# Performance work log

Measured on AMD Instinct MI355X. Metric: run time of the kernel, lower is better.

## Reference

```python
import jax, jax.numpy as jnp
import numpy as np

LOG2 = float(np.log(2.0))
CUTOFF = 10.0
N, E, H, F, G = 50000, 800000, 64, 64, 50


def ssp(x):
    # ShiftedSoftplus
    return jax.nn.softplus(x) - LOG2


def setup_inputs() -> dict:
    key = jax.random.key(0)
    ks = jax.random.split(key, 20)
    s = 0.05
    inp = {
        'x0': jax.random.normal(ks[0], (N, H), jnp.float32),
        'x1': jax.random.normal(ks[1], (N, H), jnp.float32),
        'edge_index0': jax.random.randint(ks[2], (2, E), 0, N, jnp.int32),
        'edge_index1': jax.random.randint(ks[3], (2, E), 0, N, jnp.int32),
        'edge_weight0': jax.random.uniform(ks[4], (E,), jnp.float32) * CUTOFF,
        'edge_weight1': jax.random.uniform(ks[5], (E,), jnp.float32) * CUTOFF,
        'edge_attr0': jax.random.uniform(ks[6], (E, G), jnp.float32),
        'edge_attr1': jax.random.uniform(ks[7], (E, G), jnp.float32),
        # shared filter MLP (num_gaussians -> num_filters -> num_filters)
        'mlp_w1': jax.random.normal(ks[8], (G, F), jnp.float32) * s,
        'mlp_b1': jnp.zeros((F,), jnp.float32),
        'mlp_w2': jax.random.normal(ks[9], (F, F), jnp.float32) * s,
        'mlp_b2': jnp.zeros((F,), jnp.float32),
        # per-edge-type CFConv lin1 (H->F, no bias) and lin2 (F->H, bias)
        'lin1_w0': jax.random.normal(ks[10], (H, F), jnp.float32) * s,
        'lin2_w0': jax.random.normal(ks[11], (F, H), jnp.float32) * s,
        'lin2_b0': jnp.zeros((H,), jnp.float32),
        'lin1_w1': jax.random.normal(ks[12], (H, F), jnp.float32) * s,
        'lin2_w1': jax.random.normal(ks[13], (F, H), jnp.float32) * s,
        'lin2_b1': jnp.zeros((H,), jnp.float32),
        # trailing shared linear H->H
        'lin_w': jax.random.normal(ks[14], (H, H), jnp.float32) * s,
        'lin_b': jnp.zeros((H,), jnp.float32),
    }
    return inp


def cfconv(x, ei, ew, ea, l1w, l2w, l2b, mw1, mb1, mw2, mb2):
    # cosine cutoff on distances
    C = 0.5 * (jnp.cos(ew * (jnp.pi / CUTOFF)) + 1.0)  # [E]
    # filter MLP on RBF edge attrs: Linear -> SSP -> Linear
    W = (ssp(ea @ mw1 + mb1) @ mw2 + mb2) * C[:, None]  # [E,F]
    xs = x @ l1w                                        # [N,F]
    msg = xs[ei[0]] * W                                 # gather src, modulate
    agg = jax.ops.segment_sum(msg, ei[1], num_segments=x.shape[0])  # scatter-sum to dst
    return agg @ l2w + l2b                              # [N,H]


def reference(x0, x1, edge_index0, edge_index1, edge_weight0, edge_weight1,
              edge_attr0, edge_attr1, mlp_w1, mlp_b1, mlp_w2, mlp_b2,
              lin1_w0, lin2_w0, lin2_b0, lin1_w1, lin2_w1, lin2_b1,
              lin_w, lin_b):
    h0 = cfconv(x0, edge_index0, edge_weight0, edge_attr0,
                lin1_w0, lin2_w0, lin2_b0, mlp_w1, mlp_b1, mlp_w2, mlp_b2)
    h1 = cfconv(x1, edge_index1, edge_weight1, edge_attr1,
                lin1_w1, lin2_w1, lin2_b1, mlp_w1, mlp_b1, mlp_w2, mlp_b2)
    out0 = ssp(h0) @ lin_w + lin_b
    out1 = ssp(h1) @ lin_w + lin_b
    return out0, out1
```

## Files before the change

kernel.cpp:

```cpp
#include <hip/hip_runtime.h>
#include <math.h>

#define HD 64
#define GD 50
#define HALF 32
#define PAD 36
#define EPW 64
#define WPB 2

__device__ __forceinline__ float ssp_f(float x) {
    float ax = __builtin_fabsf(x);
    float e  = __expf(-ax);
    float sp = fmaxf(x, 0.0f) + __logf(1.0f + e);
    return sp - 0.69314718055994531f;
}

__global__ void __launch_bounds__(256) xs_kernel(
        const float* __restrict__ xA, const float* __restrict__ xB,
        const float* __restrict__ wA, const float* __restrict__ wB,
        float* __restrict__ xsA, float* __restrict__ xsB,
        float* __restrict__ aggA, float* __restrict__ aggB,
        int NA, int NB) {
    const int t = blockIdx.y;
    const float* x   = t ? xB : xA;
    const float* w   = t ? wB : wA;
    float* xs  = t ? xsB : xsA;
    float* agg = t ? aggB : aggA;
    const int N = t ? NB : NA;

    int wv = threadIdx.x >> 6;
    int j  = threadIdx.x & 63;
    int n  = blockIdx.x * 4 + wv;
    __shared__ float xr[4][64];
    if (n < N) xr[wv][j] = x[(size_t)n * HD + j];
    __syncthreads();
    if (n >= N) return;
    float acc = 0.0f;
#pragma unroll
    for (int k = 0; k < HD; ++k)
        acc = fmaf(xr[wv][k], w[k * HD + j], acc);
    xs[(size_t)n * HD + j] = acc;
    agg[(size_t)n * HD + j] = 0.0f;
}

__global__ void __launch_bounds__(WPB * 64, 2) edge_kernel(
        const float* __restrict__ eaA, const float* __restrict__ eaB,
        const float* __restrict__ ewA, const float* __restrict__ ewB,
        const int* __restrict__ eiA, const int* __restrict__ eiB,
        const float* __restrict__ xsA, const float* __restrict__ xsB,
        float* __restrict__ aggA, float* __restrict__ aggB,
        const float* __restrict__ mw1, const float* __restrict__ mb1,
        const float* __restrict__ mw2, const float* __restrict__ mb2,
        int EA, int EB) {
    const int t = blockIdx.y;
    const float* ea = t ? eaB : eaA;
    const float* ew = t ? ewB : ewA;
    const int*   ei = t ? eiB : eiA;
    const float* xs = t ? xsB : xsA;
    float*      agg = t ? aggB : aggA;
    const int E = t ? EB : EA;

    if ((size_t)blockIdx.x * (WPB * EPW) >= (size_t)E) return;

    const int wv   = threadIdx.x >> 6;
    const int lane = threadIdx.x & 63;
    const long ebase = ((long)blockIdx.x * WPB + wv) * EPW;

    __shared__ float wbuf[WPB][EPW * PAD];
    __shared__ int   sdst[WPB][EPW];
    __shared__ int   ssrc[WPB][EPW];

    long e = ebase + lane;
    bool valid = e < (long)E;
    long ec = valid ? e : (long)E - 1;

    const float2* ear2 = (const float2*)(ea + ec * GD);
    float h[HD];
#pragma unroll
    for (int f = 0; f < HD; ++f) h[f] = mb1[f];
    {
        float2 v = ear2[0];
        for (int gc = 0; gc < GD / 2; ++gc) {
            int gn = gc + 1 < GD / 2 ? gc + 1 : GD / 2 - 1;
            float2 vn = ear2[gn];
            const float* wr = mw1 + 2 * gc * HD;
#pragma unroll
            for (int f = 0; f < HD; ++f) h[f] = fmaf(v.x, wr[f], h[f]);
#pragma unroll
            for (int f = 0; f < HD; ++f) h[f] = fmaf(v.y, wr[HD + f], h[f]);
            v = vn;
        }
    }

    float* hrow = &wbuf[wv][lane * PAD];
#pragma unroll
    for (int q = 0; q < HALF / 4; ++q)
        *(float4*)(hrow + 4 * q) = make_float4(h[HALF + 4*q],     h[HALF + 4*q + 1],
                                               h[HALF + 4*q + 2], h[HALF + 4*q + 3]);

    float w[HD];
#pragma unroll
    for (int j = 0; j < HD; ++j) w[j] = mb2[j];

#pragma unroll
    for (int gb = 0; gb < HALF / 4; ++gb) {
        float s0 = ssp_f(h[4*gb + 0]);
        float s1 = ssp_f(h[4*gb + 1]);
        float s2 = ssp_f(h[4*gb + 2]);
        float s3 = ssp_f(h[4*gb + 3]);
        const float* wr = mw2 + 4 * gb * HD;
#pragma unroll
        for (int j = 0; j < HD; ++j) w[j] = fmaf(s0, wr[j], w[j]);
#pragma unroll
        for (int j = 0; j < HD; ++j) w[j] = fmaf(s1, wr[HD + j], w[j]);
#pragma unroll
        for (int j = 0; j < HD; ++j) w[j] = fmaf(s2, wr[2 * HD + j], w[j]);
#pragma unroll
        for (int j = 0; j < HD; ++j) w[j] = fmaf(s3, wr[3 * HD + j], w[j]);
    }

    {
        float4 hv = *(const float4*)(hrow);
        for (int gb = 0; gb < HALF / 4; ++gb) {
            int gn = gb + 1 < HALF / 4 ? gb + 1 : HALF / 4 - 1;
            float4 hn = *(const float4*)(hrow + 4 * gn);
            float s0 = ssp_f(hv.x), s1 = ssp_f(hv.y), s2 = ssp_f(hv.z), s3 = ssp_f(hv.w);
            const float* wr = mw2 + (HALF + 4 * gb) * HD;
#pragma unroll
            for (int j = 0; j < HD; ++j) w[j] = fmaf(s0, wr[j], w[j]);
#pragma unroll
            for (int j = 0; j < HD; ++j) w[j] = fmaf(s1, wr[HD + j], w[j]);
#pragma unroll
            for (int j = 0; j < HD; ++j) w[j] = fmaf(s2, wr[2 * HD + j], w[j]);
#pragma unroll
            for (int j = 0; j < HD; ++j) w[j] = fmaf(s3, wr[3 * HD + j], w[j]);
            hv = hn;
        }
    }

    float cw = 0.5f * (__cosf(ew[ec] * 0.31415926535897931f) + 1.0f);
    if (!valid) cw = 0.0f;

    sdst[wv][lane] = ei[(size_t)E + ec];
    ssrc[wv][lane] = ei[ec];

    const int c  = lane & 31;
    const int eh = lane & 32;

#pragma unroll
    for (int q = 0; q < HALF / 4; ++q)
        *(float4*)(hrow + 4 * q) = make_float4(w[4*q] * cw,     w[4*q + 1] * cw,
                                               w[4*q + 2] * cw, w[4*q + 3] * cw);
    __syncthreads();
    float xh[EPW / 2];
#pragma unroll
    for (int k = 0; k < EPW / 2; ++k) {
        int idx = k + eh;
        int dst = sdst[wv][idx];
        int src = ssrc[wv][idx];
        const float* xp = xs + (size_t)src * HD + c;
        float xlo = xp[0];
        xh[k] = xp[HALF];
        atomicAdd(&agg[(size_t)dst * HD + c], xlo * wbuf[wv][idx * PAD + c]);
    }
    __syncthreads();

#pragma unroll
    for (int q = 0; q < HALF / 4; ++q)
        *(float4*)(hrow + 4 * q) = make_float4(w[HALF + 4*q] * cw,     w[HALF + 4*q + 1] * cw,
                                               w[HALF + 4*q + 2] * cw, w[HALF + 4*q + 3] * cw);
    __syncthreads();
#pragma unroll
    for (int k = 0; k < EPW / 2; ++k) {
        int idx = k + eh;
        int dst = sdst[wv][idx];
        atomicAdd(&agg[(size_t)dst * HD + HALF + c], xh[k] * wbuf[wv][idx * PAD + c]);
    }
}

__global__ void __launch_bounds__(256) out_kernel(
        const float* __restrict__ aggA, const float* __restrict__ aggB,
        const float* __restrict__ l2wA, const float* __restrict__ l2wB,
        const float* __restrict__ l2bA, const float* __restrict__ l2bB,
        const float* __restrict__ lw, const float* __restrict__ lb,
        float* __restrict__ outA, float* __restrict__ outB,
        int NA, int NB) {
    const int t = blockIdx.y;
    const float* agg = t ? aggB : aggA;
    const float* l2w = t ? l2wB : l2wA;
    const float* l2b = t ? l2bB : l2bA;
    float* out = t ? outB : outA;
    const int N = t ? NB : NA;

    int wv = threadIdx.x >> 6;
    int j  = threadIdx.x & 63;
    int n  = blockIdx.x * 4 + wv;
    __shared__ float buf[4][64];
    bool ok = n < N;
    if (ok) buf[wv][j] = agg[(size_t)n * HD + j];
    __syncthreads();
    float h = l2b[j];
#pragma unroll
    for (int g = 0; g < HD; ++g)
        h = fmaf(buf[wv][g], l2w[g * HD + j], h);
    h = ssp_f(h);
    __syncthreads();
    buf[wv][j] = h;
    __syncthreads();
    float o = lb[j];
#pragma unroll
    for (int g = 0; g < HD; ++g)
        o = fmaf(buf[wv][g], lw[g * HD + j], o);
    if (ok) out[(size_t)n * HD + j] = o;
}

extern "C" void kernel_launch(void* const* d_in, const int* in_sizes, int n_in,
                              void* d_out, int out_size, void* d_ws, size_t ws_size,
                              hipStream_t stream) {
    const float* x0   = (const float*)d_in[0];
    const float* x1   = (const float*)d_in[1];
    const int*   ei0  = (const int*)d_in[2];
    const int*   ei1  = (const int*)d_in[3];
    const float* ew0  = (const float*)d_in[4];
    const float* ew1  = (const float*)d_in[5];
    const float* ea0  = (const float*)d_in[6];
    const float* ea1  = (const float*)d_in[7];
    const float* mw1  = (const float*)d_in[8];
    const float* mb1  = (const float*)d_in[9];
    const float* mw2  = (const float*)d_in[10];
    const float* mb2  = (const float*)d_in[11];
    const float* l1w0 = (const float*)d_in[12];
    const float* l2w0 = (const float*)d_in[13];
    const float* l2b0 = (const float*)d_in[14];
    const float* l1w1 = (const float*)d_in[15];
    const float* l2w1 = (const float*)d_in[16];
    const float* l2b1 = (const float*)d_in[17];
    const float* lw   = (const float*)d_in[18];
    const float* lb   = (const float*)d_in[19];

    int N0 = in_sizes[0] / HD;
    int N1 = in_sizes[1] / HD;
    int E0 = in_sizes[4];
    int E1 = in_sizes[5];
    float* out = (float*)d_out;
    float* out0 = out;
    float* out1 = out + (size_t)N0 * HD;

    int Nmax = N0 > N1 ? N0 : N1;
    int Emax = E0 > E1 ? E0 : E1;
    int nodeBlocks = (Nmax + 3) / 4;
    int edgeBlocks = (Emax + WPB * EPW - 1) / (WPB * EPW);

    size_t needMerged = (size_t)(N0 + N1) * HD * 2 * sizeof(float);

    if (ws_size >= needMerged) {
        float* xs0  = (float*)d_ws;
        float* xs1  = xs0 + (size_t)N0 * HD;
        float* agg0 = xs1 + (size_t)N1 * HD;
        float* agg1 = agg0 + (size_t)N0 * HD;

        xs_kernel<<<dim3(nodeBlocks, 2), 256, 0, stream>>>(
            x0, x1, l1w0, l1w1, xs0, xs1, agg0, agg1, N0, N1);
        edge_kernel<<<dim3(edgeBlocks, 2), WPB * 64, 0, stream>>>(
            ea0, ea1, ew0, ew1, ei0, ei1, xs0, xs1, agg0, agg1,
            mw1, mb1, mw2, mb2, E0, E1);
        out_kernel<<<dim3(nodeBlocks, 2), 256, 0, stream>>>(
            agg0, agg1, l2w0, l2w1, l2b0, l2b1, lw, lb, out0, out1, N0, N1);
    } else {
        float* xs  = (float*)d_ws;
        float* agg = xs + (size_t)Nmax * HD;
        for (int t = 0; t < 2; ++t) {
            const float* x   = t ? x1 : x0;
            const int*   ei  = t ? ei1 : ei0;
            const float* ewp = t ? ew1 : ew0;
            const float* eap = t ? ea1 : ea0;
            const float* l1w = t ? l1w1 : l1w0;
            const float* l2w = t ? l2w1 : l2w0;
            const float* l2b = t ? l2b1 : l2b0;
            int N = t ? N1 : N0;
            int E = t ? E1 : E0;
            float* outp = t ? out1 : out0;
            int nb = (N + 3) / 4;
            int eb = (E + WPB * EPW - 1) / (WPB * EPW);
            xs_kernel<<<dim3(nb, 1), 256, 0, stream>>>(
                x, x, l1w, l1w, xs, xs, agg, agg, N, N);
            edge_kernel<<<dim3(eb, 1), WPB * 64, 0, stream>>>(
                eap, eap, ewp, ewp, ei, ei, xs, xs, agg, agg,
                mw1, mb1, mw2, mb2, E, E);
            out_kernel<<<dim3(nb, 1), 256, 0, stream>>>(
                agg, agg, l2w, l2w, l2b, l2b, lw, lb, outp, outp, N, N);
        }
    }
}
```

Before: 1.189 ms.

## Remap edge scatter to full-wave rows with swizzled LDS and shuffled indices

The scatter phase now has all 64 lanes handle one edge's full 64-feature row at a time, in two batches of 32 edges. Previously each half-wave handled 32 features, and xs's upper half was buffered in registers between two passes. Source and destination indices are broadcast with wave shuffles instead of being staged in shared memory. XOR swizzling of the shared filter buffer replaces padding to avoid bank conflicts. Block-wide __syncthreads are replaced by wave-local s_waitcnt, since each wave owns its buffer. The aims are fully coalesced 256-byte gathers and atomics and less barrier and register overhead. The risk is relying on in-order LDS execution within a wave instead of explicit barriers.

```diff
diff --git a/kernel.cpp b/kernel.cpp
--- a/kernel.cpp
+++ b/kernel.cpp
@@ -3,8 +3,6 @@
 
 #define HD 64
 #define GD 50
-#define HALF 32
-#define PAD 36
 #define EPW 64
 #define WPB 2
 
@@ -52,27 +50,31 @@
         const float* __restrict__ mw1, const float* __restrict__ mb1,
         const float* __restrict__ mw2, const float* __restrict__ mb2,
         int EA, int EB) {
-    const int t = blockIdx.y;
-    const float* ea = t ? eaB : eaA;
-    const float* ew = t ? ewB : ewA;
-    const int*   ei = t ? eiB : eiA;
-    const float* xs = t ? xsB : xsA;
-    float*      agg = t ? aggB : aggA;
-    const int E = t ? EB : EA;
-
-    if ((size_t)blockIdx.x * (WPB * EPW) >= (size_t)E) return;
+    const int ty = blockIdx.y;
+    const float* ea = ty ? eaB : eaA;
+    const float* ew = ty ? ewB : ewA;
+    const int*   ei = ty ? eiB : eiA;
+    const float* xs = ty ? xsB : xsA;
+    float*      agg = ty ? aggB : aggA;
+    const int E = ty ? EB : EA;
 
     const int wv   = threadIdx.x >> 6;
     const int lane = threadIdx.x & 63;
     const long ebase = ((long)blockIdx.x * WPB + wv) * EPW;
 
-    __shared__ float wbuf[WPB][EPW * PAD];
-    __shared__ int   sdst[WPB][EPW];
-    __shared__ int   ssrc[WPB][EPW];
+    __shared__ float wbuf[WPB][EPW * 32];
+    float* wb = wbuf[wv];
+
+    if (ebase >= (long)E) return;
 
     long e = ebase + lane;
     bool valid = e < (long)E;
     long ec = valid ? e : (long)E - 1;
+
+    int srcR = ei[ec];
+    int dstR = ei[(size_t)E + ec];
+    float cw = 0.5f * (__cosf(ew[ec] * 0.31415926535897931f) + 1.0f);
+    if (!valid) cw = 0.0f;
 
     const float2* ear2 = (const float2*)(ea + ec * GD);
     float h[HD];
@@ -92,18 +94,23 @@
         }
     }
 
-    float* hrow = &wbuf[wv][lane * PAD];
-#pragma unroll
-    for (int q = 0; q < HALF / 4; ++q)
-        *(float4*)(hrow + 4 * q) = make_float4(h[HALF + 4*q],     h[HALF + 4*q + 1],
-                                               h[HALF + 4*q + 2], h[HALF + 4*q + 3]);
+    {
+        float* pr = wb + lane * 32;
+        const int sw = lane & 7;
+#pragma unroll
+        for (int q = 0; q < 8; ++q)
+            *(float4*)(pr + 4 * (q ^ sw)) =
+                make_float4(h[32 + 4*q], h[32 + 4*q + 1],
+                            h[32 + 4*q + 2], h[32 + 4*q + 3]);
+    }
+    asm volatile("s_waitcnt lgkmcnt(0)" ::: "memory");
 
     float w[HD];
 #pragma unroll
     for (int j = 0; j < HD; ++j) w[j] = mb2[j];
 
 #pragma unroll
-    for (int gb = 0; gb < HALF / 4; ++gb) {
+    for (int gb = 0; gb < 8; ++gb) {
         float s0 = ssp_f(h[4*gb + 0]);
         float s1 = ssp_f(h[4*gb + 1]);
         float s2 = ssp_f(h[4*gb + 2]);
@@ -120,12 +127,14 @@
     }
 
     {
-        float4 hv = *(const float4*)(hrow);
-        for (int gb = 0; gb < HALF / 4; ++gb) {
-            int gn = gb + 1 < HALF / 4 ? gb + 1 : HALF / 4 - 1;
-            float4 hn = *(const float4*)(hrow + 4 * gn);
+        float* pr = wb + lane * 32;
+        const int sw = lane & 7;
+        float4 hv = *(const float4*)(pr + 4 * (0 ^ sw));
+        for (int gb = 0; gb < 8; ++gb) {
+            int gn = gb + 1 < 8 ? gb + 1 : 7;
+            float4 hn = *(const float4*)(pr + 4 * (gn ^ sw));
             float s0 = ssp_f(hv.x), s1 = ssp_f(hv.y), s2 = ssp_f(hv.z), s3 = ssp_f(hv.w);
-            const float* wr = mw2 + (HALF + 4 * gb) * HD;
+            const float* wr = mw2 + (32 + 4 * gb) * HD;
 #pragma unroll
             for (int j = 0; j < HD; ++j) w[j] = fmaf(s0, wr[j], w[j]);
 #pragma unroll
@@ -138,43 +147,30 @@
         }
     }
 
-    float cw = 0.5f * (__cosf(ew[ec] * 0.31415926535897931f) + 1.0f);
-    if (!valid) cw = 0.0f;
-
-    sdst[wv][lane] = ei[(size_t)E + ec];
-    ssrc[wv][lane] = ei[ec];
-
-    const int c  = lane & 31;
-    const int eh = lane & 32;
-
-#pragma unroll
-    for (int q = 0; q < HALF / 4; ++q)
-        *(float4*)(hrow + 4 * q) = make_float4(w[4*q] * cw,     w[4*q + 1] * cw,
-                                               w[4*q + 2] * cw, w[4*q + 3] * cw);
-    __syncthreads();
-    float xh[EPW / 2];
-#pragma unroll
-    for (int k = 0; k < EPW / 2; ++k) {
-        int idx = k + eh;
-        int dst = sdst[wv][idx];
-        int src = ssrc[wv][idx];
-        const float* xp = xs + (size_t)src * HD + c;
-        float xlo = xp[0];
-        xh[k] = xp[HALF];
-        atomicAdd(&agg[(size_t)dst * HD + c], xlo * wbuf[wv][idx * PAD + c]);
-    }
-    __syncthreads();
-
-#pragma unroll
-    for (int q = 0; q < HALF / 4; ++q)
-        *(float4*)(hrow + 4 * q) = make_float4(w[HALF + 4*q] * cw,     w[HALF + 4*q + 1] * cw,
-                                               w[HALF + 4*q + 2] * cw, w[HALF + 4*q + 3] * cw);
-    __syncthreads();
-#pragma unroll
-    for (int k = 0; k < EPW / 2; ++k) {
-        int idx = k + eh;
-        int dst = sdst[wv][idx];
-        atomicAdd(&agg[(size_t)dst * HD + HALF + c], xh[k] * wbuf[wv][idx * PAD + c]);
+#pragma unroll
+    for (int hb = 0; hb < 2; ++hb) {
+        if ((lane >> 5) == hb) {
+            const int r  = lane & 31;
+            const int sw = r & 7;
+            float* row = wb + r * HD;
+#pragma unroll
+            for (int q = 0; q < 16; ++q)
+                *(float4*)(row + 4 * (q ^ sw)) =
+                    make_float4(w[4*q] * cw,     w[4*q + 1] * cw,
+                                w[4*q + 2] * cw, w[4*q + 3] * cw);
+        }
+        asm volatile("s_waitcnt lgkmcnt(0)" ::: "memory");
+
+#pragma unroll
+        for (int k = 0; k < 32; ++k) {
+            const int et = hb * 32 + k;
+            int s = __shfl(srcR, et);
+            int d = __shfl(dstR, et);
+            float xv = xs[(size_t)s * HD + lane];
+            float wk = wb[k * HD + (lane ^ ((k & 7) << 2))];
+            atomicAdd(&agg[(size_t)d * HD + lane], xv * wk);
+        }
+        asm volatile("s_waitcnt lgkmcnt(0)" ::: "memory");
     }
 }
 
```

Result: slower. 1.271 ms (+6.8%).
